# Performance work log

Measured on AMD Instinct MI355X. Metric: run time of the kernel, lower is better.

Reference implementation:

```python
import jax, jax.numpy as jnp
import numpy as np

S, R, CM, H, CA, CZ = 128, 256, 256, 8, 32, 128


def _ln(x, w, b):
    mu = x.mean(-1, keepdims=True)
    var = x.var(-1, keepdims=True)
    return (x - mu) * jax.lax.rsqrt(var + 1e-5) * w + b


def setup_inputs() -> dict:
    key = jax.random.key(0)
    ks = jax.random.split(key, 20)
    n = lambda i, shape: jax.random.normal(ks[i], shape, jnp.float32) * 0.05
    return {
        "m": jax.random.normal(ks[0], (S, R, CM), jnp.float32),
        "m_mask": jnp.ones((S, R), jnp.float32),
        "z": jax.random.normal(ks[1], (R, R, CZ), jnp.float32),
        "row_ln_w": jnp.ones((CM,)), "row_ln_b": jnp.zeros((CM,)),
        "row_z_ln_w": jnp.ones((CZ,)), "row_z_ln_b": jnp.zeros((CZ,)),
        "row_wq": n(2, (CM, H * CA)), "row_wk": n(3, (CM, H * CA)), "row_wv": n(4, (CM, H * CA)),
        "row_wb": n(5, (CZ, H)),
        "row_wg": n(6, (CM, H * CA)), "row_bg": jnp.zeros((H * CA,)),
        "row_wo": n(7, (H * CA, CM)), "row_bo": jnp.zeros((CM,)),
        "col_ln_w": jnp.ones((CM,)), "col_ln_b": jnp.zeros((CM,)),
        "col_wq": n(8, (CM, H * CA)), "col_wk": n(9, (CM, H * CA)), "col_wv": n(10, (CM, H * CA)),
        "col_wg": n(11, (CM, H * CA)), "col_bg": jnp.zeros((H * CA,)),
        "col_wo": n(12, (H * CA, CM)), "col_bo": jnp.zeros((CM,)),
        "tr_ln_w": jnp.ones((CM,)), "tr_ln_b": jnp.zeros((CM,)),
        "tr_w1": n(13, (CM, 4 * CM)), "tr_b1": jnp.zeros((4 * CM,)),
        "tr_w2": n(14, (4 * CM, CM)), "tr_b2": jnp.zeros((CM,)),
    }


def _row_atten(m, m_mask, z, ln_w, ln_b, z_ln_w, z_ln_b, wq, wk, wv, wb, wg, bg, wo, bo):
    # MSA row attention with pair bias: attend over residues within each sequence row.
    x = _ln(m, ln_w, ln_b)                                   # [s,r,cm]
    q = (x @ wq).reshape(S, R, H, CA) * (CA ** -0.5)
    k = (x @ wk).reshape(S, R, H, CA)
    v = (x @ wv).reshape(S, R, H, CA)
    pair_bias = jnp.transpose(_ln(z, z_ln_w, z_ln_b) @ wb, (2, 0, 1))  # [h,r,r]
    mask_bias = (m_mask - 1.0)[:, None, None, :] * 1e9       # [s,1,1,r] over keys
    logits = jnp.einsum('sqhc,skhc->shqk', q, k) + pair_bias[None] + mask_bias
    a = jax.nn.softmax(logits, axis=-1)
    o = jnp.einsum('shqk,skhc->sqhc', a, v)
    g = jax.nn.sigmoid(x @ wg + bg).reshape(S, R, H, CA)
    return (g * o).reshape(S, R, H * CA) @ wo + bo


def _col_atten(m, m_mask, ln_w, ln_b, wq, wk, wv, wg, bg, wo, bo):
    # MSA column attention: attend over sequences within each residue column.
    x = _ln(m, ln_w, ln_b)                                   # [s,r,cm]
    q = (x @ wq).reshape(S, R, H, CA) * (CA ** -0.5)
    k = (x @ wk).reshape(S, R, H, CA)
    v = (x @ wv).reshape(S, R, H, CA)
    mask_bias = (jnp.transpose(m_mask) - 1.0)[:, None, None, :] * 1e9  # [r,1,1,s]
    logits = jnp.einsum('qrhc,krhc->rhqk', q, k) + mask_bias
    a = jax.nn.softmax(logits, axis=-1)
    o = jnp.einsum('rhqk,krhc->qrhc', a, v)
    g = jax.nn.sigmoid(x @ wg + bg).reshape(S, R, H, CA)
    return (g * o).reshape(S, R, H * CA) @ wo + bo


def _transition(m, ln_w, ln_b, w1, b1, w2, b2):
    x = _ln(m, ln_w, ln_b)
    return jax.nn.relu(x @ w1 + b1) @ w2 + b2


def reference(m, m_mask, z,
              row_ln_w, row_ln_b, row_z_ln_w, row_z_ln_b,
              row_wq, row_wk, row_wv, row_wb, row_wg, row_bg, row_wo, row_bo,
              col_ln_w, col_ln_b, col_wq, col_wk, col_wv, col_wg, col_bg, col_wo, col_bo,
              tr_ln_w, tr_ln_b, tr_w1, tr_b1, tr_w2, tr_b2):
    m = m + _row_atten(m, m_mask, z, row_ln_w, row_ln_b, row_z_ln_w, row_z_ln_b,
                       row_wq, row_wk, row_wv, row_wb, row_wg, row_bg, row_wo, row_bo)
    m = m + _col_atten(m, m_mask, col_ln_w, col_ln_b, col_wq, col_wk, col_wv,
                       col_wg, col_bg, col_wo, col_bo)
    m = m + _transition(m, tr_ln_w, tr_ln_b, tr_w1, tr_b1, tr_w2, tr_b2)
    return m
```

## Files before the change

kernel.cpp:

```cpp
#include <hip/hip_runtime.h>
#include <stdint.h>

#define S_ 128
#define R_ 256
#define CM_ 256
#define H_ 8
#define CA_ 32
#define CZ_ 128

typedef unsigned short u16;
typedef __bf16 bf16x8 __attribute__((ext_vector_type(8)));
typedef float f32x4 __attribute__((ext_vector_type(4)));

#define LOG2E 1.4426950408889634f

__device__ __forceinline__ float bf2f(u16 u){ unsigned v = ((unsigned)u) << 16; float f; __builtin_memcpy(&f, &v, 4); return f; }
__device__ __forceinline__ u16 f2bf(float f){ __bf16 h = (__bf16)f; u16 u; __builtin_memcpy(&u, &h, 2); return u; }
__device__ __forceinline__ unsigned pkbf(float lo, float hi){
  unsigned r; asm("v_cvt_pk_bf16_f32 %0, %1, %2" : "=v"(r) : "v"(lo), "v"(hi)); return r;
}
__device__ __forceinline__ float fexp2(float x){
  float r; asm("v_exp_f32 %0, %1" : "=v"(r) : "v"(x)); return r;
}

__device__ __forceinline__ void gl16(const void* g, void* l){
  __builtin_amdgcn_global_load_lds((const __attribute__((address_space(1))) void*)g,
                                   (__attribute__((address_space(3))) void*)l, 16, 0, 0);
}

struct WSrc { const float* p[12]; };
__global__ __launch_bounds__(256) void transpose_all(WSrc srcs, u16* __restrict__ dst){
  int b = blockIdx.x, t = threadIdx.x;
  int job, idx;
  if(b < 2560){ job = b >> 8; idx = ((b & 255) << 8) + t; }
  else if(b < 3584){ job = 10; idx = ((b - 2560) << 8) + t; }
  else { job = 11; idx = ((b - 3584) << 8) + t; }
  int K = (job == 11) ? 1024 : 256;
  int N = (job == 10) ? 1024 : 256;
  int off;
  if(job < 10) off = job * 65536;
  else if(job == 10) off = 655360;
  else off = 917504;
  int k = idx / N, n = idx - k * N;
  float sc = (job == 0 || job == 5) ? (0.17677669529663687f * LOG2E) : 1.f;
  dst[off + n * K + k] = f2bf(srcs.p[job][idx] * sc);
}

__global__ __launch_bounds__(256) void ln_kernel(const float* __restrict__ in, const float* __restrict__ w,
                          const float* __restrict__ b, u16* __restrict__ out){
  int wv = threadIdx.x >> 6, lane = threadIdx.x & 63;
  long long row = (long long)blockIdx.x * 4 + wv;
  float4 v = ((const float4*)(in + row * CM_))[lane];
  float s = v.x + v.y + v.z + v.w;
  for(int mo = 32; mo; mo >>= 1) s += __shfl_xor(s, mo, 64);
  float mu = s * (1.f / CM_);
  float dx = v.x - mu, dy = v.y - mu, dz = v.z - mu, dw = v.w - mu;
  float s2 = dx * dx + dy * dy + dz * dz + dw * dw;
  for(int mo = 32; mo; mo >>= 1) s2 += __shfl_xor(s2, mo, 64);
  float rstd = rsqrtf(s2 * (1.f / CM_) + 1e-5f);
  float4 w4 = ((const float4*)w)[lane];
  float4 b4 = ((const float4*)b)[lane];
  ushort4 st;
  st.x = f2bf(dx * rstd * w4.x + b4.x);
  st.y = f2bf(dy * rstd * w4.y + b4.y);
  st.z = f2bf(dz * rstd * w4.z + b4.z);
  st.w = f2bf(dw * rstd * w4.w + b4.w);
  *(ushort4*)(out + row * CM_ + lane * 4) = st;
}

__global__ __launch_bounds__(256) void pair_bias_kernel(const float* __restrict__ z, const float* __restrict__ lnw,
                                 const float* __restrict__ lnb, const float* __restrict__ wb,
                                 u16* __restrict__ pb){
  __shared__ __attribute__((aligned(16))) unsigned char Xl[32 * 256];
  __shared__ __attribute__((aligned(16))) unsigned char Wl[16 * 256];
  const int t = threadIdx.x;
  const int wv = t >> 6, lane = t & 63, l15 = lane & 15, l4 = lane >> 4;
  const int r0 = blockIdx.x * 32;

  if(t < 128){
    const float4* wr = (const float4*)(wb + t * 8);
    float4 a = wr[0], bq = wr[1];
    u16 vals[8] = {f2bf(a.x), f2bf(a.y), f2bf(a.z), f2bf(a.w),
                   f2bf(bq.x), f2bf(bq.y), f2bf(bq.z), f2bf(bq.w)};
    #pragma unroll
    for(int n = 0; n < 8; n++){
      *(u16*)(Wl + ((n * 256 + t * 2) ^ ((n & 7) << 4))) = vals[n];
      *(u16*)(Wl + (((n + 8) * 256 + t * 2) ^ ((n & 7) << 4))) = 0;
    }
  }
  {
    int row = wv * 8 + (lane >> 3);
    int c0 = (lane & 7) * 16;
    const float4* rp = (const float4*)(z + (long long)(r0 + row) * CZ_ + c0);
    float4 v0 = rp[0], v1 = rp[1], v2 = rp[2], v3 = rp[3];
    float s = v0.x + v0.y + v0.z + v0.w + v1.x + v1.y + v1.z + v1.w
            + v2.x + v2.y + v2.z + v2.w + v3.x + v3.y + v3.z + v3.w;
    s += __shfl_xor(s, 1, 64); s += __shfl_xor(s, 2, 64); s += __shfl_xor(s, 4, 64);
    float mu = s * (1.f / CZ_);
    float d[16] = {v0.x - mu, v0.y - mu, v0.z - mu, v0.w - mu,
                   v1.x - mu, v1.y - mu, v1.z - mu, v1.w - mu,
                   v2.x - mu, v2.y - mu, v2.z - mu, v2.w - mu,
                   v3.x - mu, v3.y - mu, v3.z - mu, v3.w - mu};
    float s2 = 0.f;
    #pragma unroll
    for(int i = 0; i < 16; i++) s2 += d[i] * d[i];
    s2 += __shfl_xor(s2, 1, 64); s2 += __shfl_xor(s2, 2, 64); s2 += __shfl_xor(s2, 4, 64);
    float rstd = rsqrtf(s2 * (1.f / CZ_) + 1e-5f);
    const float4* wp = (const float4*)(lnw + c0);
    const float4* bp = (const float4*)(lnb + c0);
    float x[16];
    #pragma unroll
    for(int i = 0; i < 4; i++){
      float4 w4 = wp[i], b4 = bp[i];
      x[i * 4 + 0] = d[i * 4 + 0] * rstd * w4.x + b4.x;
      x[i * 4 + 1] = d[i * 4 + 1] * rstd * w4.y + b4.y;
      x[i * 4 + 2] = d[i * 4 + 2] * rstd * w4.z + b4.z;
      x[i * 4 + 3] = d[i * 4 + 3] * rstd * w4.w + b4.w;
    }
    uint4 p0, p1;
    p0.x = pkbf(x[0], x[1]);  p0.y = pkbf(x[2], x[3]);
    p0.z = pkbf(x[4], x[5]);  p0.w = pkbf(x[6], x[7]);
    p1.x = pkbf(x[8], x[9]);  p1.y = pkbf(x[10], x[11]);
    p1.z = pkbf(x[12], x[13]); p1.w = pkbf(x[14], x[15]);
    *(uint4*)(Xl + ((row * 256 + c0 * 2) ^ ((row & 7) << 4))) = p0;
    *(uint4*)(Xl + ((row * 256 + c0 * 2 + 16) ^ ((row & 7) << 4))) = p1;
  }
  __syncthreads();
  if(wv < 2){
    f32x4 acc = {0.f, 0.f, 0.f, 0.f};
    #pragma unroll
    for(int ks = 0; ks < 4; ks++){
      int rowA = wv * 16 + l15;
      bf16x8 a = *(const bf16x8*)(Xl + ((rowA * 256 + l4 * 16 + ks * 64) ^ ((rowA & 7) << 4)));
      bf16x8 b = *(const bf16x8*)(Wl + ((l15 * 256 + l4 * 16 + ks * 64) ^ ((l15 & 7) << 4)));
      acc = __builtin_amdgcn_mfma_f32_16x16x32_bf16(a, b, acc, 0, 0, 0);
    }
    if(l15 < 8){
      #pragma unroll
      for(int r = 0; r < 4; r++){
        int rowg = r0 + wv * 16 + l4 * 4 + r;
        int q = rowg >> 8, k = rowg & 255;
        int off = (((l15 * 16 + (q >> 4)) * 16 + (k >> 4)) << 10)
                + ((((q >> 2) & 3) * 16 + (k & 15)) << 2) + (q & 3);
        pb[off] = f2bf(acc[r] * LOG2E);
      }
    }
  }
}

template<bool HAS_BIAS, bool HAS_SIG, bool RELU, bool RES, bool F32OUT>
__global__ __launch_bounds__(256) void gemm128(
    const u16* __restrict__ A, const u16* __restrict__ Wt,
    const float* __restrict__ bias, const float* __restrict__ res,
    void* __restrict__ outv, int M, int N, int K, int sigStart){
  __shared__ __attribute__((aligned(16))) unsigned char Ab[16384];
  __shared__ __attribute__((aligned(16))) unsigned char Bb[16384];
  const int t = threadIdx.x;
  const int wv = t >> 6, lane = t & 63, l15 = lane & 15, l4 = lane >> 4;
  const int wm = wv >> 1, wn = wv & 1;
  const unsigned flat = blockIdx.y * gridDim.x + blockIdx.x;
  const unsigned NB = gridDim.x, mper = gridDim.y >> 3;
  const unsigned xcd = flat & 7, j = flat >> 3;
  const unsigned n_blk = j % NB, m_blk = xcd * mper + j / NB;
  const long long m0 = (long long)m_blk * 128;
  const int n0 = n_blk * 128;
  const int srow = t >> 3;
  const int ksw  = ((t & 7) ^ (srow & 7)) * 8;
  const u16* Ag = A  + (m0 + srow) * (long long)K + ksw;
  const u16* Bg = Wt + (long long)(n0 + srow) * K + ksw;
  f32x4 acc[4][4] = {};
  for(int kk = 0; kk < K; kk += 64){
    #pragma unroll
    for(int i = 0; i < 4; i++){
      gl16(Ag + (long long)i * 32 * K + kk, Ab + wv * 1024 + lane * 16 + i * 4096);
      gl16(Bg + (long long)i * 32 * K + kk, Bb + wv * 1024 + lane * 16 + i * 4096);
    }
    asm volatile("s_waitcnt vmcnt(0)" ::: "memory");
    __syncthreads();
    #pragma unroll
    for(int kh = 0; kh < 2; kh++){
      bf16x8 af[4], bq[4];
      #pragma unroll
      for(int mt = 0; mt < 4; mt++){
        int rr = wm * 64 + mt * 16 + l15;
        af[mt] = *(const bf16x8*)(Ab + rr * 128 + ((kh * 64 + l4 * 16) ^ ((rr & 7) << 4)));
      }
      #pragma unroll
      for(int nt = 0; nt < 4; nt++){
        int rr = wn * 64 + nt * 16 + l15;
        bq[nt] = *(const bf16x8*)(Bb + rr * 128 + ((kh * 64 + l4 * 16) ^ ((rr & 7) << 4)));
      }
      #pragma unroll
      for(int mt = 0; mt < 4; mt++)
        #pragma unroll
        for(int nt = 0; nt < 4; nt++)
          acc[mt][nt] = __builtin_amdgcn_mfma_f32_16x16x32_bf16(af[mt], bq[nt], acc[mt][nt], 0, 0, 0);
    }
    __syncthreads();
  }
  float bnt[4]; bool sg[4];
  #pragma unroll
  for(int nt = 0; nt < 4; nt++){
    int ncol = n0 + wn * 64 + nt * 16 + l15;
    bnt[nt] = 0.f; sg[nt] = false;
    if(HAS_BIAS){
      if(HAS_SIG){ sg[nt] = (ncol >= sigStart); bnt[nt] = sg[nt] ? bias[ncol - sigStart] : 0.f; }
      else bnt[nt] = bias[ncol];
    }
  }
  #pragma unroll
  for(int mt = 0; mt < 4; mt++){
    #pragma unroll
    for(int r = 0; r < 4; r++){
      long long mrow = m0 + wm * 64 + mt * 16 + l4 * 4 + r;
      #pragma unroll
      for(int nt = 0; nt < 4; nt++){
        int ncol = n0 + wn * 64 + nt * 16 + l15;
        float v = acc[mt][nt][r] + bnt[nt];
        if(HAS_SIG){ if(sg[nt]) v = 1.f / (1.f + __expf(-v)); }
        if(RELU) v = v > 0.f ? v : 0.f;
        if(RES)  v += res[mrow * N + ncol];
        if(F32OUT) ((float*)outv)[mrow * N + ncol] = v;
        else       ((u16*)outv)[mrow * N + ncol] = f2bf(v);
      }
    }
  }
}

template<int L, bool HAS_BIAS>
__global__ __launch_bounds__(256) void atten_kernel(
    const u16* __restrict__ qg, const u16* __restrict__ kg, const u16* __restrict__ vg,
    const u16* __restrict__ gg, const u16* __restrict__ pb, const float* __restrict__ mask,
    u16* __restrict__ og,
    long long obase_mul, long long tstride, long long obase_o, long long ostride,
    long long mbase_mul, int mstride){
  __shared__ __attribute__((aligned(16))) unsigned char smem[L * 128 + 8192];
  unsigned char* Kl = smem;
  unsigned char* Vt = smem + L * 64;
  unsigned char* Pl = smem + L * 128;

  const int t = threadIdx.x;
  const int wv = t >> 6, lane = t & 63, l15 = lane & 15, l4 = lane >> 4;
  const int h = blockIdx.x & 7;
  const int outer = blockIdx.x >> 3;
  const long long base  = (long long)outer * obase_mul + h * CA_;
  const long long baseo = (long long)outer * obase_o  + h * CA_;
  const long long mb = (long long)outer * mbase_mul;
  const int KT = L / 16, NC = L / 64;

  #pragma unroll
  for(int j = 0; j < L * 4; j += 256){
    int cid = j + t;
    int row = cid >> 2, ko = cid & 3;
    int4 kv = *(const int4*)(kg + base + (long long)row * tstride + ko * 8);
    *(int4*)(Kl + ((row * 64 + ko * 16) ^ ((row & 7) << 4))) = kv;
  }
  if(t < L){
    __attribute__((aligned(16))) u16 tmp[32];
    const u16* vp = vg + base + (long long)t * tstride;
    #pragma unroll
    for(int j2 = 0; j2 < 4; j2++) ((int4*)tmp)[j2] = *(const int4*)(vp + j2 * 8);
    int kp = (t >> 6) * 64 + (t & 15) * 4 + ((t >> 4) & 3);
    #pragma unroll
    for(int c = 0; c < 32; c++)
      *(u16*)(Vt + (((c * L + kp) * 2) ^ ((c & 7) << 4))) = tmp[c];
  }
  __syncthreads();

  float mskb[L / 16];
  #pragma unroll
  for(int kt = 0; kt < KT; kt++)
    mskb[kt] = (mask[mb + (long long)(kt * 16 + l15) * mstride] - 1.f) * (1e9f * LOG2E);

  unsigned char* Pw = Pl + wv * 2048;
  const int NQ = L / 4;
  #pragma unroll
  for(int qt = 0; qt < NQ / 16; qt++){
    const int qrow0 = wv * NQ + qt * 16;
    bf16x8 aq = *(const bf16x8*)(qg + base + (long long)(qrow0 + l15) * tstride + l4 * 8);
    f32x4 lac[L / 16];
    #pragma unroll
    for(int kt = 0; kt < KT; kt++){
      int kr = kt * 16 + l15;
      bf16x8 bk = *(const bf16x8*)(Kl + ((kr * 64 + l4 * 16) ^ ((kr & 7) << 4)));
      f32x4 zz = {0.f, 0.f, 0.f, 0.f};
      lac[kt] = __builtin_amdgcn_mfma_f32_16x16x32_bf16(aq, bk, zz, 0, 0, 0);
    }
    const u16* tile = HAS_BIAS ? (pb + (((h * 16 + (qrow0 >> 4)) * 16) << 10) + lane * 4) : nullptr;
    float sm[4] = {1e-30f, 1e-30f, 1e-30f, 1e-30f};
    #pragma unroll
    for(int kt = 0; kt < KT; kt++){
      float mm = mskb[kt];
      if(HAS_BIAS){
        ushort4 b4 = *(const ushort4*)(tile + (kt << 10));
        lac[kt][0] = fexp2(lac[kt][0] + mm + bf2f(b4.x));
        lac[kt][1] = fexp2(lac[kt][1] + mm + bf2f(b4.y));
        lac[kt][2] = fexp2(lac[kt][2] + mm + bf2f(b4.z));
        lac[kt][3] = fexp2(lac[kt][3] + mm + bf2f(b4.w));
      } else {
        #pragma unroll
        for(int r = 0; r < 4; r++) lac[kt][r] = fexp2(lac[kt][r] + mm);
      }
      #pragma unroll
      for(int r = 0; r < 4; r++) sm[r] += lac[kt][r];
    }
    #pragma unroll
    for(int mo = 1; mo < 16; mo <<= 1)
      #pragma unroll
      for(int r = 0; r < 4; r++) sm[r] += __shfl_xor(sm[r], mo, 64);
    float inv[4];
    #pragma unroll
    for(int r = 0; r < 4; r++) inv[r] = 1.f / sm[r];
    f32x4 oac[2] = {{0,0,0,0},{0,0,0,0}};
    #pragma unroll
    for(int ch = 0; ch < NC; ch++){
      asm volatile("" ::: "memory");
      #pragma unroll
      for(int r = 0; r < 4; r++){
        int qp = l4 * 4 + r;
        uint2 pk2;
        pk2.x = pkbf(lac[ch * 4 + 0][r], lac[ch * 4 + 1][r]);
        pk2.y = pkbf(lac[ch * 4 + 2][r], lac[ch * 4 + 3][r]);
        *(uint2*)(Pw + qp * 128 + ((l15 * 8) ^ ((qp & 7) << 4))) = pk2;
      }
      asm volatile("s_waitcnt lgkmcnt(0)" ::: "memory");
      #pragma unroll
      for(int ksl = 0; ksl < 2; ksl++){
        bf16x8 ap = *(const bf16x8*)(Pw + l15 * 128 + ((ksl * 64 + l4 * 16) ^ ((l15 & 7) << 4)));
        #pragma unroll
        for(int ct = 0; ct < 2; ct++){
          int c = ct * 16 + l15;
          bf16x8 bv = *(const bf16x8*)(Vt + (((c * L + ch * 64 + ksl * 32 + l4 * 8) * 2) ^ ((c & 7) << 4)));
          oac[ct] = __builtin_amdgcn_mfma_f32_16x16x32_bf16(ap, bv, oac[ct], 0, 0, 0);
        }
      }
    }
    #pragma unroll
    for(int ct = 0; ct < 2; ct++)
      #pragma unroll
      for(int r = 0; r < 4; r++){
        int qi = qrow0 + l4 * 4 + r, c = ct * 16 + l15;
        float g = bf2f(gg[base + (long long)qi * tstride + c]);
        og[baseo + (long long)qi * ostride + c] = f2bf(oac[ct][r] * inv[r] * g);
      }
  }
}

extern "C" void kernel_launch(void* const* d_in, const int* in_sizes, int n_in,
                              void* d_out, int out_size, void* d_ws, size_t ws_size,
                              hipStream_t stream){
  const float* m        = (const float*)d_in[0];
  const float* m_mask   = (const float*)d_in[1];
  const float* z        = (const float*)d_in[2];
  const float* row_ln_w = (const float*)d_in[3];
  const float* row_ln_b = (const float*)d_in[4];
  const float* row_z_ln_w = (const float*)d_in[5];
  const float* row_z_ln_b = (const float*)d_in[6];
  const float* row_bg   = (const float*)d_in[12];
  const float* row_bo   = (const float*)d_in[14];
  const float* col_ln_w = (const float*)d_in[15];
  const float* col_ln_b = (const float*)d_in[16];
  const float* col_bg   = (const float*)d_in[21];
  const float* col_bo   = (const float*)d_in[23];
  const float* tr_ln_w  = (const float*)d_in[24];
  const float* tr_ln_b  = (const float*)d_in[25];
  const float* tr_b1    = (const float*)d_in[27];
  const float* tr_b2    = (const float*)d_in[29];
  float* out = (float*)d_out;
  char* ws = (char*)d_ws;

  u16* bx  = (u16*)ws;
  u16* fq  = bx + 8388608;
  u16* t_o = fq + 33554432;
  u16* pb  = t_o + 8388608;
  u16* wt  = pb + 2097152;

  WSrc srcs;
  srcs.p[0] = (const float*)d_in[7];
  srcs.p[1] = (const float*)d_in[8];
  srcs.p[2] = (const float*)d_in[9];
  srcs.p[3] = (const float*)d_in[11];
  srcs.p[4] = (const float*)d_in[13];
  srcs.p[5] = (const float*)d_in[17];
  srcs.p[6] = (const float*)d_in[18];
  srcs.p[7] = (const float*)d_in[19];
  srcs.p[8] = (const float*)d_in[20];
  srcs.p[9] = (const float*)d_in[22];
  srcs.p[10] = (const float*)d_in[26];
  srcs.p[11] = (const float*)d_in[28];

  dim3 b256(256);
  transpose_all<<<dim3(4608), b256, 0, stream>>>(srcs, wt);
  pair_bias_kernel<<<dim3(2048), b256, 0, stream>>>(z, row_z_ln_w, row_z_ln_b,
                                                    (const float*)d_in[10], pb);

  ln_kernel<<<dim3(8192), b256, 0, stream>>>(m, row_ln_w, row_ln_b, bx);
  gemm128<true,true,false,false,false><<<dim3(8,256), b256, 0, stream>>>(
      bx, wt, row_bg, nullptr, fq, 32768, 1024, 256, 768);
  atten_kernel<256,true><<<dim3(1024), b256, 0, stream>>>(
      fq, fq + 256, fq + 512, fq + 768, pb, m_mask, t_o,
      262144, 1024, 65536, 256, 256, 1);
  gemm128<true,false,false,true,true><<<dim3(2,256), b256, 0, stream>>>(
      t_o, wt + 262144, row_bo, m, out, 32768, 256, 256, 0);

  ln_kernel<<<dim3(8192), b256, 0, stream>>>(out, col_ln_w, col_ln_b, bx);
  gemm128<true,true,false,false,false><<<dim3(8,256), b256, 0, stream>>>(
      bx, wt + 327680, col_bg, nullptr, fq, 32768, 1024, 256, 768);
  atten_kernel<128,false><<<dim3(2048), b256, 0, stream>>>(
      fq, fq + 256, fq + 512, fq + 768, nullptr, m_mask, t_o,
      1024, 262144, 256, 65536, 1, 256);
  gemm128<true,false,false,true,true><<<dim3(2,256), b256, 0, stream>>>(
      t_o, wt + 589824, col_bo, out, out, 32768, 256, 256, 0);

  ln_kernel<<<dim3(8192), b256, 0, stream>>>(out, tr_ln_w, tr_ln_b, bx);
  gemm128<true,false,true,false,false><<<dim3(8,256), b256, 0, stream>>>(
      bx, wt + 655360, tr_b1, nullptr, fq, 32768, 1024, 256, 0);
  gemm128<true,false,false,true,true><<<dim3(2,256), b256, 0, stream>>>(
      fq, wt + 917504, tr_b2, out, out, 32768, 256, 1024, 0);
}
```

Before: 281.7 us.

## Keep intermediate residual stream in bf16 and split attention query blocks

The intermediate MSA residual stream after the row and column attention stages is now stored in bf16 rather than fp32. The layernorm and GEMM epilogue kernels are templated to read bf16 inputs and residuals, which cuts the bytes moved between stages. The attention kernels also split each (outer, head) query range across two blocks, doubling the grid to improve occupancy at the cost of loading K/V twice. Keeping the residual in bf16 lowers its precision, which may loosen accuracy.

```diff
diff --git a/kernel.cpp b/kernel.cpp
--- a/kernel.cpp
+++ b/kernel.cpp
@@ -46,15 +46,23 @@
   dst[off + n * K + k] = f2bf(srcs.p[job][idx] * sc);
 }
 
-__global__ __launch_bounds__(256) void ln_kernel(const float* __restrict__ in, const float* __restrict__ w,
+template<bool BF16IN>
+__global__ __launch_bounds__(256) void ln_kernel(const void* __restrict__ inv, const float* __restrict__ w,
                           const float* __restrict__ b, u16* __restrict__ out){
   int wv = threadIdx.x >> 6, lane = threadIdx.x & 63;
   long long row = (long long)blockIdx.x * 4 + wv;
-  float4 v = ((const float4*)(in + row * CM_))[lane];
-  float s = v.x + v.y + v.z + v.w;
+  float vx, vy, vz, vw;
+  if(BF16IN){
+    ushort4 v4 = ((const ushort4*)((const u16*)inv + row * CM_))[lane];
+    vx = bf2f(v4.x); vy = bf2f(v4.y); vz = bf2f(v4.z); vw = bf2f(v4.w);
+  } else {
+    float4 v4 = ((const float4*)((const float*)inv + row * CM_))[lane];
+    vx = v4.x; vy = v4.y; vz = v4.z; vw = v4.w;
+  }
+  float s = vx + vy + vz + vw;
   for(int mo = 32; mo; mo >>= 1) s += __shfl_xor(s, mo, 64);
   float mu = s * (1.f / CM_);
-  float dx = v.x - mu, dy = v.y - mu, dz = v.z - mu, dw = v.w - mu;
+  float dx = vx - mu, dy = vy - mu, dz = vz - mu, dw = vw - mu;
   float s2 = dx * dx + dy * dy + dz * dz + dw * dw;
   for(int mo = 32; mo; mo >>= 1) s2 += __shfl_xor(s2, mo, 64);
   float rstd = rsqrtf(s2 * (1.f / CM_) + 1e-5f);
@@ -148,10 +156,10 @@
   }
 }
 
-template<bool HAS_BIAS, bool HAS_SIG, bool RELU, bool RES, bool F32OUT>
+template<bool HAS_BIAS, bool HAS_SIG, bool RELU, int RESMODE, bool F32OUT>
 __global__ __launch_bounds__(256) void gemm128(
     const u16* __restrict__ A, const u16* __restrict__ Wt,
-    const float* __restrict__ bias, const float* __restrict__ res,
+    const float* __restrict__ bias, const void* __restrict__ res,
     void* __restrict__ outv, int M, int N, int K, int sigStart){
   __shared__ __attribute__((aligned(16))) unsigned char Ab[16384];
   __shared__ __attribute__((aligned(16))) unsigned char Bb[16384];
@@ -219,7 +227,8 @@
         float v = acc[mt][nt][r] + bnt[nt];
         if(HAS_SIG){ if(sg[nt]) v = 1.f / (1.f + __expf(-v)); }
         if(RELU) v = v > 0.f ? v : 0.f;
-        if(RES)  v += res[mrow * N + ncol];
+        if(RESMODE == 1) v += ((const float*)res)[mrow * N + ncol];
+        if(RESMODE == 2) v += bf2f(((const u16*)res)[mrow * N + ncol]);
         if(F32OUT) ((float*)outv)[mrow * N + ncol] = v;
         else       ((u16*)outv)[mrow * N + ncol] = f2bf(v);
       }
@@ -227,7 +236,7 @@
   }
 }
 
-template<int L, bool HAS_BIAS>
+template<int L, int SPLIT, bool HAS_BIAS>
 __global__ __launch_bounds__(256) void atten_kernel(
     const u16* __restrict__ qg, const u16* __restrict__ kg, const u16* __restrict__ vg,
     const u16* __restrict__ gg, const u16* __restrict__ pb, const float* __restrict__ mask,
@@ -242,11 +251,13 @@
   const int t = threadIdx.x;
   const int wv = t >> 6, lane = t & 63, l15 = lane & 15, l4 = lane >> 4;
   const int h = blockIdx.x & 7;
-  const int outer = blockIdx.x >> 3;
+  const int g2 = blockIdx.x >> 3;
+  const int sp = g2 % SPLIT;
+  const int outer = g2 / SPLIT;
   const long long base  = (long long)outer * obase_mul + h * CA_;
   const long long baseo = (long long)outer * obase_o  + h * CA_;
   const long long mb = (long long)outer * mbase_mul;
-  const int KT = L / 16, NC = L / 64;
+  const int KT = L / 16, NC = L / 64, QB = L / SPLIT;
 
   #pragma unroll
   for(int j = 0; j < L * 4; j += 256){
@@ -273,10 +284,9 @@
     mskb[kt] = (mask[mb + (long long)(kt * 16 + l15) * mstride] - 1.f) * (1e9f * LOG2E);
 
   unsigned char* Pw = Pl + wv * 2048;
-  const int NQ = L / 4;
   #pragma unroll
-  for(int qt = 0; qt < NQ / 16; qt++){
-    const int qrow0 = wv * NQ + qt * 16;
+  for(int qt = 0; qt < QB / 64; qt++){
+    const int qrow0 = sp * QB + wv * (QB / 4) + qt * 16;
     bf16x8 aq = *(const bf16x8*)(qg + base + (long long)(qrow0 + l15) * tstride + l4 * 8);
     f32x4 lac[L / 16];
     #pragma unroll
@@ -374,6 +384,8 @@
   u16* t_o = fq + 33554432;
   u16* pb  = t_o + 8388608;
   u16* wt  = pb + 2097152;
+  u16* m2  = fq;
+  u16* h1  = fq + 8388608;
 
   WSrc srcs;
   srcs.p[0] = (const float*)d_in[7];
@@ -394,27 +406,27 @@
   pair_bias_kernel<<<dim3(2048), b256, 0, stream>>>(z, row_z_ln_w, row_z_ln_b,
                                                     (const float*)d_in[10], pb);
 
-  ln_kernel<<<dim3(8192), b256, 0, stream>>>(m, row_ln_w, row_ln_b, bx);
-  gemm128<true,true,false,false,false><<<dim3(8,256), b256, 0, stream>>>(
+  ln_kernel<false><<<dim3(8192), b256, 0, stream>>>(m, row_ln_w, row_ln_b, bx);
+  gemm128<true,true,false,0,false><<<dim3(8,256), b256, 0, stream>>>(
       bx, wt, row_bg, nullptr, fq, 32768, 1024, 256, 768);
-  atten_kernel<256,true><<<dim3(1024), b256, 0, stream>>>(
+  atten_kernel<256,2,true><<<dim3(2048), b256, 0, stream>>>(
       fq, fq + 256, fq + 512, fq + 768, pb, m_mask, t_o,
       262144, 1024, 65536, 256, 256, 1);
-  gemm128<true,false,false,true,true><<<dim3(2,256), b256, 0, stream>>>(
-      t_o, wt + 262144, row_bo, m, out, 32768, 256, 256, 0);
-
-  ln_kernel<<<dim3(8192), b256, 0, stream>>>(out, col_ln_w, col_ln_b, bx);
-  gemm128<true,true,false,false,false><<<dim3(8,256), b256, 0, stream>>>(
-      bx, wt + 327680, col_bg, nullptr, fq, 32768, 1024, 256, 768);
-  atten_kernel<128,false><<<dim3(2048), b256, 0, stream>>>(
+  gemm128<true,false,false,1,false><<<dim3(2,256), b256, 0, stream>>>(
+      t_o, wt + 262144, row_bo, m, bx, 32768, 256, 256, 0);
+
+  ln_kernel<true><<<dim3(8192), b256, 0, stream>>>(bx, col_ln_w, col_ln_b, t_o);
+  gemm128<true,true,false,0,false><<<dim3(8,256), b256, 0, stream>>>(
+      t_o, wt + 327680, col_bg, nullptr, fq, 32768, 1024, 256, 768);
+  atten_kernel<128,2,false><<<dim3(4096), b256, 0, stream>>>(
       fq, fq + 256, fq + 512, fq + 768, nullptr, m_mask, t_o,
       1024, 262144, 256, 65536, 1, 256);
-  gemm128<true,false,false,true,true><<<dim3(2,256), b256, 0, stream>>>(
-      t_o, wt + 589824, col_bo, out, out, 32768, 256, 256, 0);
-
-  ln_kernel<<<dim3(8192), b256, 0, stream>>>(out, tr_ln_w, tr_ln_b, bx);
-  gemm128<true,false,true,false,false><<<dim3(8,256), b256, 0, stream>>>(
-      bx, wt + 655360, tr_b1, nullptr, fq, 32768, 1024, 256, 0);
-  gemm128<true,false,false,true,true><<<dim3(2,256), b256, 0, stream>>>(
-      fq, wt + 917504, tr_b2, out, out, 32768, 256, 1024, 0);
-}
+  gemm128<true,false,false,2,false><<<dim3(2,256), b256, 0, stream>>>(
+      t_o, wt + 589824, col_bo, bx, m2, 32768, 256, 256, 0);
+
+  ln_kernel<true><<<dim3(8192), b256, 0, stream>>>(m2, tr_ln_w, tr_ln_b, bx);
+  gemm128<true,false,true,0,false><<<dim3(8,256), b256, 0, stream>>>(
+      bx, wt + 655360, tr_b1, nullptr, h1, 32768, 1024, 256, 0);
+  gemm128<true,false,false,2,true><<<dim3(2,256), b256, 0, stream>>>(
+      h1, wt + 917504, tr_b2, m2, out, 32768, 256, 1024, 0);
+}
```

Measured after the change: 283.5 us. No clear change (+0.7%).
